# Kernel optimization log

Hardware: AMD Instinct MI355X
Metric: run time of the kernel (lower is better)

The kernel has to match this reference:

```python
import jax, jax.numpy as jnp
import numpy as np
jax.config.update("jax_enable_x64", True)

PAD_ID = -1
NUM_DISCRETE = 128  # args.n_discrete_size

def _lexsort3(v):
    # torch code: stable argsort by x, then y, then z -> final key order z (primary), y, x.
    # numpy/jax lexsort: last key is primary, and it is stable.
    idx = jnp.lexsort((v[:, 0], v[:, 1], v[:, 2]))
    return v[idx], idx

def setup_inputs() -> dict:
    key = jax.random.key(0)
    k1, k2 = jax.random.split(key)
    B, NV, NF = 32, 32768, 65536
    vertices = jax.random.normal(k1, (B, NV, 3), dtype=jnp.float32)
    faces = jax.random.randint(k2, (B, NF, 3), 0, NV, dtype=jnp.int64)
    n_pad = NF // 10
    faces = faces.at[:, NF - n_pad:, :].set(PAD_ID)
    return {"vertices": vertices, "faces": faces}

def reference(vertices, faces):
    B, NV, _ = vertices.shape
    # normalize_vertices reduces over dim 0 (which is the BATCH dim here) - faithful to source
    mn = vertices.min(axis=0)
    mx = vertices.max(axis=0)
    center = (mn + mx) * 0.5
    longest = (mx - mn).max()
    v = (vertices - center) / longest
    # batched lexicographic sort of vertices
    sorted_v, sort_idx = jax.vmap(_lexsort3)(v)
    # inverse permutation (inv[sort_idx] = arange  <=>  argsort of a permutation)
    inv = jnp.argsort(sort_idx, axis=1)  # (B, NV)
    # torch indexes inverse_mapping[faces] with pad -1 wrapping to NV-1
    wrapped = jnp.mod(faces, NV)
    reindexed = jax.vmap(lambda m, f: m[f])(inv, wrapped)  # (B, NF, 3)
    sorted_faces, _ = jax.vmap(_lexsort3)(reindexed)
    # face mask: all three vertex ids != pad
    face_mask = jnp.all(faces != PAD_ID, axis=-1)  # (B, NF)
    face_np = jnp.where(face_mask[..., None], faces, 0)
    # gather vertex coords per face: (B, NF, 3verts, 3coords). The torch code
    # materializes a (b,nf,nv,3) repeat then gathers; we gather directly.
    face_coords = jax.vmap(lambda vv, ff: vv[ff])(sorted_v, face_np)
    # discretize into [-1, 1] -> [0, 127]
    t = (face_coords + 1.0) * 0.5 * NUM_DISCRETE - 0.5
    dq = jnp.clip(jnp.round(t).astype(jnp.int64), 0, NUM_DISCRETE - 1)
    codes = jnp.where(face_mask[..., None, None], dq, PAD_ID)
    input_ids = codes.reshape(B, -1)
    attention_mask = (input_ids != PAD_ID).astype(jnp.float32)
    ph = jnp.full((B, 1), PAD_ID, dtype=input_ids.dtype)
    input_ids = jnp.concatenate([ph, input_ids, ph], axis=1)
    attention_mask = jnp.concatenate([ph.astype(jnp.float32), attention_mask, ph.astype(jnp.float32)], axis=1)
    return input_ids, attention_mask, codes, dq, sorted_faces
```

## Files before the change

kernel.cpp:

```cpp
#include <hip/hip_runtime.h>
#include <stdint.h>

#define BATCH 32
#define NV 32768
#define NF 65536
#define PCOUNT (NV*3)


__device__ __forceinline__ unsigned fenc(float f){
  unsigned u = __float_as_uint(f);
  return (u & 0x80000000u) ? ~u : (u | 0x80000000u);
}
__device__ __forceinline__ float fdec(unsigned e){
  unsigned u = (e & 0x80000000u) ? (e & 0x7FFFFFFFu) : ~e;
  return __uint_as_float(u);
}

__global__ void kminmax(const float* __restrict__ vert, float* __restrict__ center,
                        unsigned* __restrict__ longestBits){
  int p = blockIdx.x*256 + threadIdx.x;
  float mn = 3.4e38f, mx = -3.4e38f;
  #pragma unroll
  for (int b = 0; b < BATCH; ++b) {
    float v = vert[(size_t)b*PCOUNT + p];
    mn = fminf(mn, v); mx = fmaxf(mx, v);
  }
  center[p] = __fadd_rn(mn, mx) * 0.5f;
  float r = __fsub_rn(mx, mn);
  for (int off = 32; off > 0; off >>= 1) r = fmaxf(r, __shfl_down(r, off, 64));
  if ((threadIdx.x & 63) == 0) atomicMax(longestBits, __float_as_uint(r));
}

__device__ __forceinline__ bool less4(uint4 a, uint4 b){
  if (a.x != b.x) return a.x < b.x;
  if (a.y != b.y) return a.y < b.y;
  if (a.z != b.z) return a.z < b.z;
  return a.w < b.w;
}
__device__ __forceinline__ bool less2(uint2 a, uint2 b){
  if (a.y != b.y) return a.y < b.y;
  return a.x < b.x;
}

__device__ __forceinline__ int split64v(const uint4* __restrict__ A,
                                        const uint4* __restrict__ B,
                                        int k, int L){
  int lo = k - L; if (lo < 0) lo = 0;
  int hi = k < L ? k : L;
  int lane = threadIdx.x & 63;
  while (lo < hi){
    int n = hi - lo;
    int pos = lo + (int)(((long long)n * lane) >> 6);
    bool pred = less4(A[pos], B[k-1-pos]);
    unsigned long long m = __ballot(pred);
    int t = __popcll(m);
    if (t == 0){ hi = lo; break; }
    int pl = lo + (int)(((long long)n * (t-1)) >> 6);
    int nh = (t == 64) ? hi : (lo + (int)(((long long)n * t) >> 6));
    lo = pl + 1; hi = nh;
  }
  return lo;
}
__device__ __forceinline__ int split64f(const uint2* __restrict__ A,
                                        const uint2* __restrict__ B,
                                        int k, int L){
  int lo = k - L; if (lo < 0) lo = 0;
  int hi = k < L ? k : L;
  int lane = threadIdx.x & 63;
  while (lo < hi){
    int n = hi - lo;
    int pos = lo + (int)(((long long)n * lane) >> 6);
    bool pred = less2(A[pos], B[k-1-pos]);
    unsigned long long m = __ballot(pred);
    int t = __popcll(m);
    if (t == 0){ hi = lo; break; }
    int pl = lo + (int)(((long long)n * (t-1)) >> 6);
    int nh = (t == 64) ? hi : (lo + (int)(((long long)n * t) >> 6));
    lo = pl + 1; hi = nh;
  }
  return lo;
}

#define VT 4096
#define FT 8192
#define SWV(i) ((i) ^ (((i) >> 3) & 7))
#define SWF(i) ((i) ^ (((i) >> 4) & 15))

__global__ __launch_bounds__(1024) void klocalv(const float* __restrict__ vert,
                                                const float* __restrict__ center,
                                                const unsigned* __restrict__ longestBits,
                                                uint4* __restrict__ S){
  __shared__ uint4 sh[VT];
  int blockBase = blockIdx.x * VT;
  float L = __uint_as_float(*longestBits);
  float rl = __fdiv_rn(1.0f, L);
  for (int i = threadIdx.x; i < VT; i += 1024){
    int id = blockBase + i;
    int vi = id & (NV-1);
    size_t vb = (size_t)(id >> 15)*PCOUNT + (size_t)vi*3;
    float nx = __fsub_rn(vert[vb+0], center[vi*3+0]);
    float ny = __fsub_rn(vert[vb+1], center[vi*3+1]);
    float nz = __fsub_rn(vert[vb+2], center[vi*3+2]);
    float x = __fmul_rn(nx, rl);
    float y = __fmul_rn(ny, rl);
    float z = __fmul_rn(nz, rl);
    uint4 s; s.x = fenc(z); s.y = fenc(y); s.z = fenc(x); s.w = (unsigned)vi;
    sh[SWV(i)] = s;
  }
  __syncthreads();
  int t = threadIdx.x;
  int k0 = t * 4;
  uint4 v[4];
  #pragma unroll
  for (int e = 0; e < 4; ++e) v[e] = sh[SWV(k0 + e)];
  #pragma unroll
  for (int k = 2; k <= 4; k <<= 1){
    #pragma unroll
    for (int j = k >> 1; j > 0; j >>= 1){
      #pragma unroll
      for (int i = 0; i < 4; ++i){
        int l = i ^ j;
        if (l > i){
          bool up = ((i & k) == 0);
          bool sw = up ? less4(v[l], v[i]) : less4(v[i], v[l]);
          if (sw){ uint4 tmp = v[i]; v[i] = v[l]; v[l] = tmp; }
        }
      }
    }
  }
  #pragma unroll
  for (int e = 0; e < 4; ++e) sh[SWV(k0 + e)] = v[e];
  __syncthreads();
  for (int w = 4; w < VT; w <<= 1){
    int base = k0 & ~(2*w - 1);
    int ko = k0 - base;
    int lo = ko - w; if (lo < 0) lo = 0;
    int hi = ko < w ? ko : w;
    while (lo < hi){
      int mid = (lo + hi) >> 1;
      if (less4(sh[SWV(base + mid)], sh[SWV(base + w + ko-1-mid)])) lo = mid + 1; else hi = mid;
    }
    int i = lo, j = ko - lo;
    uint4 m[4];
    #pragma unroll
    for (int e = 0; e < 4; ++e){
      bool takeA = (j >= w) || (i < w && less4(sh[SWV(base + i)], sh[SWV(base + w + j)]));
      m[e] = takeA ? sh[SWV(base + i)] : sh[SWV(base + w + j)];
      if (takeA) ++i; else ++j;
    }
    __syncthreads();
    #pragma unroll
    for (int e = 0; e < 4; ++e) sh[SWV(k0 + e)] = m[e];
    __syncthreads();
  }
  uint4* basep = S + (size_t)blockBase;
  for (int i = threadIdx.x; i < VT; i += 1024) basep[i] = sh[SWV(i)];
}

__global__ __launch_bounds__(256) void kmergev(const uint4* __restrict__ src,
                                               uint4* __restrict__ dst, int L){
  __shared__ uint4 sh[1024];
  __shared__ int sAB[2];
  int gid = blockIdx.x;
  int b = gid >> 5, c = gid & 31;
  const uint4* base = src + ((size_t)b << 15);
  uint4* obase = dst + ((size_t)b << 15);
  int co = c * 1024;
  int pair = co / (2*L);
  int ko = co - pair*2*L;
  const uint4* A = base + (size_t)pair*2*L;
  const uint4* B = A + L;
  uint4* O = obase + (size_t)pair*2*L + ko;
  int wv = threadIdx.x >> 6;
  if (wv < 2){
    int s = split64v(A, B, ko + wv*1024, L);
    if ((threadIdx.x & 63) == 0) sAB[wv] = s;
  }
  __syncthreads();
  int aStart = sAB[0];
  int na = sAB[1] - aStart;
  int nb = 1024 - na;
  int bStart = ko - aStart;
  for (int i = threadIdx.x; i < 1024; i += 256)
    sh[i] = (i < na) ? A[aStart + i] : B[bStart + (i - na)];
  __syncthreads();
  int k0 = threadIdx.x * 4;
  int lo = k0 - nb; if (lo < 0) lo = 0;
  int hi = k0 < na ? k0 : na;
  while (lo < hi){
    int mid = (lo + hi) >> 1;
    if (less4(sh[mid], sh[na + k0-1-mid])) lo = mid + 1; else hi = mid;
  }
  int i = lo, j = k0 - lo;
  #pragma unroll
  for (int e = 0; e < 4; ++e){
    bool takeA = (j >= nb) || (i < na && less4(sh[i], sh[na + j]));
    uint4 v = takeA ? sh[i] : sh[na + j];
    if (takeA) ++i; else ++j;
    O[k0 + e] = v;
  }
}

__global__ __launch_bounds__(256) void kmergevQ(const uint4* __restrict__ src,
                                                int* __restrict__ inv,
                                                unsigned* __restrict__ Q){
  #pragma clang fp contract(off)
  __shared__ uint4 sh[1024];
  __shared__ int sAB[2];
  const int L = 16384;
  int gid = blockIdx.x;
  int b = gid >> 5, c = gid & 31;
  const uint4* A = src + ((size_t)b << 15);
  const uint4* B = A + L;
  int ko = c * 1024;
  int wv = threadIdx.x >> 6;
  if (wv < 2){
    int s = split64v(A, B, ko + wv*1024, L);
    if ((threadIdx.x & 63) == 0) sAB[wv] = s;
  }
  __syncthreads();
  int aStart = sAB[0];
  int na = sAB[1] - aStart;
  int nb = 1024 - na;
  int bStart = ko - aStart;
  for (int i = threadIdx.x; i < 1024; i += 256)
    sh[i] = (i < na) ? A[aStart + i] : B[bStart + (i - na)];
  __syncthreads();
  int k0 = threadIdx.x * 4;
  int lo = k0 - nb; if (lo < 0) lo = 0;
  int hi = k0 < na ? k0 : na;
  while (lo < hi){
    int mid = (lo + hi) >> 1;
    if (less4(sh[mid], sh[na + k0-1-mid])) lo = mid + 1; else hi = mid;
  }
  int i = lo, j = k0 - lo;
  #pragma unroll
  for (int e = 0; e < 4; ++e){
    bool takeA = (j >= nb) || (i < na && less4(sh[i], sh[na + j]));
    uint4 s = takeA ? sh[i] : sh[na + j];
    if (takeA) ++i; else ++j;
    int pos = ko + k0 + e;
    inv[(b<<15) + (int)s.w] = pos;
    float cco[3]; cco[0] = fdec(s.z); cco[1] = fdec(s.y); cco[2] = fdec(s.x);
    unsigned qw = 0;
    #pragma unroll
    for (int cc = 0; cc < 3; ++cc){
      float tt = ((cco[cc] + 1.0f) * 0.5f) * 128.0f - 0.5f;
      float rq = rintf(tt);
      int qi = (int)rq;
      qi = qi < 0 ? 0 : (qi > 127 ? 127 : qi);
      qw |= ((unsigned)qi) << (8*cc);
    }
    Q[(b<<15) + pos] = qw;
  }
}

__global__ __launch_bounds__(1024) void klocalfB(const int* __restrict__ faces,
                                                 const int* __restrict__ inv,
                                                 const unsigned* __restrict__ Qt,
                                                 uint2* __restrict__ F,
                                                 float* __restrict__ out){
  __shared__ __align__(16) uint2 sh[FT];
  float* shq = (float*)sh;
  float* shm = ((float*)sh) + 9216;
  int p = blockIdx.x;
  int l = ((p & 7) << 5) | (p >> 3);
  int blockBase = l * FT;
  int b = blockBase >> 16;
  const int* invb = inv + (b << 15);
  const unsigned* Qb = Qt + (b << 15);
  int t = threadIdx.x;
  uint2 v[8];
  #pragma unroll 8
  for (int c = 0; c < 8; ++c){
    int i = c*1024 + t;
    int id = blockBase + i;
    int f = id & (NF-1);
    size_t fb = (size_t)id*3;
    int f0 = faces[fb+0], f1 = faces[fb+1], f2 = faces[fb+2];
    bool mask = (f0 != -1) & (f1 != -1) & (f2 != -1);
    unsigned r0 = (unsigned)invb[f0 & (NV-1)];
    unsigned r1 = (unsigned)invb[f1 & (NV-1)];
    unsigned r2 = (unsigned)invb[f2 & (NV-1)];
    v[c].x = (r0 << 15) | (unsigned)f;
    v[c].y = (r2 << 15) | r1;
    unsigned qw0 = Qb[mask ? f0 : 0];
    unsigned qw1 = Qb[mask ? f1 : 0];
    unsigned qw2 = Qb[mask ? f2 : 0];
    shm[t] = mask ? 1.0f : 0.0f;
    shq[t*9+0] = (float)( qw0        & 255u);
    shq[t*9+1] = (float)((qw0 >> 8 ) & 255u);
    shq[t*9+2] = (float)((qw0 >> 16) & 255u);
    shq[t*9+3] = (float)( qw1        & 255u);
    shq[t*9+4] = (float)((qw1 >> 8 ) & 255u);
    shq[t*9+5] = (float)((qw1 >> 16) & 255u);
    shq[t*9+6] = (float)( qw2        & 255u);
    shq[t*9+7] = (float)((qw2 >> 8 ) & 255u);
    shq[t*9+8] = (float)((qw2 >> 16) & 255u);
    __syncthreads();
    float4* cp = (float4*)(out + 37748864 + ((size_t)blockBase + c*1024)*9);
    float4* dp = (float4*)(out + 56623232 + ((size_t)blockBase + c*1024)*9);
    for (int r = t; r < 2304; r += 1024){
      int e0 = r*4;
      float4 q = *(const float4*)&shq[e0];
      float m0 = shm[(unsigned)(e0  )/9u];
      float m1 = shm[(unsigned)(e0+1)/9u];
      float m2 = shm[(unsigned)(e0+2)/9u];
      float m3 = shm[(unsigned)(e0+3)/9u];
      float4 cv;
      cv.x = m0 != 0.0f ? q.x : -1.0f;
      cv.y = m1 != 0.0f ? q.y : -1.0f;
      cv.z = m2 != 0.0f ? q.z : -1.0f;
      cv.w = m3 != 0.0f ? q.w : -1.0f;
      cp[r] = cv;
      dp[r] = q;
    }
    size_t fi = (size_t)(blockBase & (NF-1)) + (size_t)c*1024;
    size_t idsBase  = (size_t)b*589826 + 1 + fi*9;
    size_t attnBase = 18874432 + idsBase;
    #pragma unroll
    for (int r = 0; r < 9; ++r){
      int idx = r*1024 + t;
      float q = shq[idx];
      float m = shm[(unsigned)idx/9u];
      out[idsBase + idx]  = m != 0.0f ? q : -1.0f;
      out[attnBase + idx] = m;
    }
    __syncthreads();
  }
  if ((blockBase & (NF-1)) == 0 && t == 0){
    out[(size_t)b*589826]                     = -1.0f;
    out[(size_t)b*589826 + 589825]            = -1.0f;
    out[18874432 + (size_t)b*589826]          = -1.0f;
    out[18874432 + (size_t)b*589826 + 589825] = -1.0f;
  }
  #pragma unroll
  for (int k = 2; k <= 8; k <<= 1){
    #pragma unroll
    for (int j = k >> 1; j > 0; j >>= 1){
      #pragma unroll
      for (int i = 0; i < 8; ++i){
        int l2 = i ^ j;
        if (l2 > i){
          bool up = ((i & k) == 0);
          bool sw = up ? less2(v[l2], v[i]) : less2(v[i], v[l2]);
          if (sw){ uint2 tmp = v[i]; v[i] = v[l2]; v[l2] = tmp; }
        }
      }
    }
  }
  int k0 = t * 8;
  #pragma unroll
  for (int e = 0; e < 8; ++e) sh[SWF(k0 + e)] = v[e];
  __syncthreads();
  for (int w = 8; w < FT; w <<= 1){
    int base = k0 & ~(2*w - 1);
    int ko = k0 - base;
    int lo = ko - w; if (lo < 0) lo = 0;
    int hi = ko < w ? ko : w;
    while (lo < hi){
      int mid = (lo + hi) >> 1;
      if (less2(sh[SWF(base + mid)], sh[SWF(base + w + ko-1-mid)])) lo = mid + 1; else hi = mid;
    }
    int i = lo, j = ko - lo;
    uint2 m[8];
    #pragma unroll
    for (int e = 0; e < 8; ++e){
      bool takeA = (j >= w) || (i < w && less2(sh[SWF(base + i)], sh[SWF(base + w + j)]));
      m[e] = takeA ? sh[SWF(base + i)] : sh[SWF(base + w + j)];
      if (takeA) ++i; else ++j;
    }
    __syncthreads();
    #pragma unroll
    for (int e = 0; e < 8; ++e) sh[SWF(k0 + e)] = m[e];
    __syncthreads();
  }
  uint2* basep = F + (size_t)blockBase;
  for (int i = threadIdx.x; i < FT; i += 1024) basep[i] = sh[SWF(i)];
}

__global__ __launch_bounds__(256) void kmergef(const uint2* __restrict__ src,
                                               uint2* __restrict__ dst, int L){
  __shared__ uint2 sh[1024];
  __shared__ int sAB[2];
  int gid = blockIdx.x;
  int b = gid >> 6, c = gid & 63;
  const uint2* base = src + ((size_t)b << 16);
  uint2* obase = dst + ((size_t)b << 16);
  int co = c * 1024;
  int pair = co / (2*L);
  int ko = co - pair*2*L;
  const uint2* A = base + (size_t)pair*2*L;
  const uint2* B = A + L;
  uint2* O = obase + (size_t)pair*2*L + ko;
  int wv = threadIdx.x >> 6;
  if (wv < 2){
    int s = split64f(A, B, ko + wv*1024, L);
    if ((threadIdx.x & 63) == 0) sAB[wv] = s;
  }
  __syncthreads();
  int aStart = sAB[0];
  int na = sAB[1] - aStart;
  int nb = 1024 - na;
  int bStart = ko - aStart;
  for (int i = threadIdx.x; i < 1024; i += 256)
    sh[i] = (i < na) ? A[aStart + i] : B[bStart + (i - na)];
  __syncthreads();
  int k0 = threadIdx.x * 4;
  int lo = k0 - nb; if (lo < 0) lo = 0;
  int hi = k0 < na ? k0 : na;
  while (lo < hi){
    int mid = (lo + hi) >> 1;
    if (less2(sh[mid], sh[na + k0-1-mid])) lo = mid + 1; else hi = mid;
  }
  int i = lo, j = k0 - lo;
  #pragma unroll
  for (int e = 0; e < 4; ++e){
    bool takeA = (j >= nb) || (i < na && less2(sh[i], sh[na + j]));
    uint2 v = takeA ? sh[i] : sh[na + j];
    if (takeA) ++i; else ++j;
    O[k0 + e] = v;
  }
}

__global__ __launch_bounds__(256) void kmergefOut(const uint2* __restrict__ src,
                                                  float* __restrict__ out){
  __shared__ __align__(16) float shf[3072];
  __shared__ int sAB[2];
  uint2* sh = (uint2*)shf;
  const int L = 32768;
  int gid = blockIdx.x;
  int b = gid >> 6, c = gid & 63;
  const uint2* A = src + ((size_t)b << 16);
  const uint2* B = A + L;
  int ko = c * 1024;
  int wv = threadIdx.x >> 6;
  if (wv < 2){
    int s = split64f(A, B, ko + wv*1024, L);
    if ((threadIdx.x & 63) == 0) sAB[wv] = s;
  }
  __syncthreads();
  int aStart = sAB[0];
  int na = sAB[1] - aStart;
  int nb = 1024 - na;
  int bStart = ko - aStart;
  for (int i = threadIdx.x; i < 1024; i += 256)
    sh[i] = (i < na) ? A[aStart + i] : B[bStart + (i - na)];
  __syncthreads();
  int k0 = threadIdx.x * 4;
  int lo = k0 - nb; if (lo < 0) lo = 0;
  int hi = k0 < na ? k0 : na;
  while (lo < hi){
    int mid = (lo + hi) >> 1;
    if (less2(sh[mid], sh[na + k0-1-mid])) lo = mid + 1; else hi = mid;
  }
  int i = lo, j = k0 - lo;
  uint2 v[4];
  #pragma unroll
  for (int e = 0; e < 4; ++e){
    bool takeA = (j >= nb) || (i < na && less2(sh[i], sh[na + j]));
    v[e] = takeA ? sh[i] : sh[na + j];
    if (takeA) ++i; else ++j;
  }
  __syncthreads();
  #pragma unroll
  for (int e = 0; e < 4; ++e){
    int o = (k0 + e) * 3;
    shf[o+0] = (float)(v[e].x >> 15);
    shf[o+1] = (float)(v[e].y & 0x7FFFu);
    shf[o+2] = (float)(v[e].y >> 15);
  }
  __syncthreads();
  size_t basef = 75497600 + ((size_t)b*65536 + (size_t)ko)*3;
  for (int q = threadIdx.x; q < 3072; q += 256) out[basef + q] = shf[q];
}

extern "C" void kernel_launch(void* const* d_in, const int* in_sizes, int n_in,
                              void* d_out, int out_size, void* d_ws, size_t ws_size,
                              hipStream_t stream){
  const float* vert  = (const float*)d_in[0];
  const int*   faces = (const int*)d_in[1];
  float* out = (float*)d_out;

  uint4*    S           = (uint4*)d_ws;
  uint4*    S2          = (uint4*)((char*)d_ws + 16777216);
  uint2*    FKa         = (uint2*)((char*)d_ws + 16777216);
  unsigned* Q           = (unsigned*)((char*)d_ws + 16777216);
  uint2*    FKb         = (uint2*)d_ws;
  int*      inv         = (int*)((char*)d_ws + 33554432);
  float*    center      = (float*)((char*)d_ws + 37748736);
  unsigned* longestBits = (unsigned*)((char*)d_ws + 38141952);

  hipMemsetAsync(longestBits, 0, 4, stream);
  kminmax<<<PCOUNT/256, 256, 0, stream>>>(vert, center, longestBits);

  klocalv<<<BATCH*(NV/VT), 1024, 0, stream>>>(vert, center, longestBits, S);
  kmergev<<<BATCH*32, 256, 0, stream>>>(S,  S2, 4096);
  kmergev<<<BATCH*32, 256, 0, stream>>>(S2, S,  8192);
  kmergevQ<<<BATCH*32, 256, 0, stream>>>(S, inv, Q);

  klocalfB<<<BATCH*(NF/FT), 1024, 0, stream>>>(faces, inv, Q, FKb, out);

  kmergef<<<BATCH*64, 256, 0, stream>>>(FKb, FKa, 8192);
  kmergef<<<BATCH*64, 256, 0, stream>>>(FKa, FKb, 16384);
  kmergefOut<<<BATCH*64, 256, 0, stream>>>(FKb, out);
}
```

Measured before the change: 595.1 us.

## Stage per-wave output chunks in LDS to drop block-wide barriers

Each wavefront now owns a private 640-float LDS slice and handles 64 contiguous faces per iteration, instead of the whole block sharing one staging buffer for 1024 faces. The two __syncthreads per chunk are replaced by an lgkmcnt wait and a scheduling barrier, because a wave only reads what it wrote itself. One barrier is added before the sort phase reuses the same LDS. This changes which faces each thread holds before the local sort and relies on wave-level ordering of LDS accesses, which is a correctness risk.

```diff
diff --git a/kernel.cpp b/kernel.cpp
--- a/kernel.cpp
+++ b/kernel.cpp
@@ -5,6 +5,8 @@
 #define NV 32768
 #define NF 65536
 #define PCOUNT (NV*3)
+
+typedef float f32x4 __attribute__((ext_vector_type(4)));
 
 
 __device__ __forceinline__ unsigned fenc(float f){
@@ -261,8 +263,6 @@
                                                  uint2* __restrict__ F,
                                                  float* __restrict__ out){
   __shared__ __align__(16) uint2 sh[FT];
-  float* shq = (float*)sh;
-  float* shm = ((float*)sh) + 9216;
   int p = blockIdx.x;
   int l = ((p & 7) << 5) | (p >> 3);
   int blockBase = l * FT;
@@ -270,10 +270,13 @@
   const int* invb = inv + (b << 15);
   const unsigned* Qb = Qt + (b << 15);
   int t = threadIdx.x;
+  int wv = t >> 6, ln = t & 63;
+  float* wq = ((float*)sh) + wv*640;
+  float* wm = wq + 576;
   uint2 v[8];
-  #pragma unroll 8
-  for (int c = 0; c < 8; ++c){
-    int i = c*1024 + t;
+  #pragma unroll
+  for (int e = 0; e < 8; ++e){
+    int i = wv*512 + e*64 + ln;
     int id = blockBase + i;
     int f = id & (NF-1);
     size_t fb = (size_t)id*3;
@@ -282,32 +285,34 @@
     unsigned r0 = (unsigned)invb[f0 & (NV-1)];
     unsigned r1 = (unsigned)invb[f1 & (NV-1)];
     unsigned r2 = (unsigned)invb[f2 & (NV-1)];
-    v[c].x = (r0 << 15) | (unsigned)f;
-    v[c].y = (r2 << 15) | r1;
+    v[e].x = (r0 << 15) | (unsigned)f;
+    v[e].y = (r2 << 15) | r1;
     unsigned qw0 = Qb[mask ? f0 : 0];
     unsigned qw1 = Qb[mask ? f1 : 0];
     unsigned qw2 = Qb[mask ? f2 : 0];
-    shm[t] = mask ? 1.0f : 0.0f;
-    shq[t*9+0] = (float)( qw0        & 255u);
-    shq[t*9+1] = (float)((qw0 >> 8 ) & 255u);
-    shq[t*9+2] = (float)((qw0 >> 16) & 255u);
-    shq[t*9+3] = (float)( qw1        & 255u);
-    shq[t*9+4] = (float)((qw1 >> 8 ) & 255u);
-    shq[t*9+5] = (float)((qw1 >> 16) & 255u);
-    shq[t*9+6] = (float)( qw2        & 255u);
-    shq[t*9+7] = (float)((qw2 >> 8 ) & 255u);
-    shq[t*9+8] = (float)((qw2 >> 16) & 255u);
-    __syncthreads();
-    float4* cp = (float4*)(out + 37748864 + ((size_t)blockBase + c*1024)*9);
-    float4* dp = (float4*)(out + 56623232 + ((size_t)blockBase + c*1024)*9);
-    for (int r = t; r < 2304; r += 1024){
+    wm[ln] = mask ? 1.0f : 0.0f;
+    wq[ln*9+0] = (float)( qw0        & 255u);
+    wq[ln*9+1] = (float)((qw0 >> 8 ) & 255u);
+    wq[ln*9+2] = (float)((qw0 >> 16) & 255u);
+    wq[ln*9+3] = (float)( qw1        & 255u);
+    wq[ln*9+4] = (float)((qw1 >> 8 ) & 255u);
+    wq[ln*9+5] = (float)((qw1 >> 16) & 255u);
+    wq[ln*9+6] = (float)( qw2        & 255u);
+    wq[ln*9+7] = (float)((qw2 >> 8 ) & 255u);
+    wq[ln*9+8] = (float)((qw2 >> 16) & 255u);
+    asm volatile("s_waitcnt lgkmcnt(0)" ::: "memory");
+    __builtin_amdgcn_sched_barrier(0);
+    size_t chunkF = (size_t)blockBase + (size_t)wv*512 + (size_t)e*64;
+    f32x4* cp = (f32x4*)(out + 37748864 + chunkF*9);
+    f32x4* dp = (f32x4*)(out + 56623232 + chunkF*9);
+    for (int r = ln; r < 144; r += 64){
       int e0 = r*4;
-      float4 q = *(const float4*)&shq[e0];
-      float m0 = shm[(unsigned)(e0  )/9u];
-      float m1 = shm[(unsigned)(e0+1)/9u];
-      float m2 = shm[(unsigned)(e0+2)/9u];
-      float m3 = shm[(unsigned)(e0+3)/9u];
-      float4 cv;
+      f32x4 q = *(const f32x4*)&wq[e0];
+      float m0 = wm[(unsigned)(e0  )/9u];
+      float m1 = wm[(unsigned)(e0+1)/9u];
+      float m2 = wm[(unsigned)(e0+2)/9u];
+      float m3 = wm[(unsigned)(e0+3)/9u];
+      f32x4 cv;
       cv.x = m0 != 0.0f ? q.x : -1.0f;
       cv.y = m1 != 0.0f ? q.y : -1.0f;
       cv.z = m2 != 0.0f ? q.z : -1.0f;
@@ -315,18 +320,17 @@
       cp[r] = cv;
       dp[r] = q;
     }
-    size_t fi = (size_t)(blockBase & (NF-1)) + (size_t)c*1024;
+    size_t fi = chunkF & (NF-1);
     size_t idsBase  = (size_t)b*589826 + 1 + fi*9;
     size_t attnBase = 18874432 + idsBase;
     #pragma unroll
     for (int r = 0; r < 9; ++r){
-      int idx = r*1024 + t;
-      float q = shq[idx];
-      float m = shm[(unsigned)idx/9u];
+      int idx = r*64 + ln;
+      float q = wq[idx];
+      float m = wm[(unsigned)idx/9u];
       out[idsBase + idx]  = m != 0.0f ? q : -1.0f;
       out[attnBase + idx] = m;
     }
-    __syncthreads();
   }
   if ((blockBase & (NF-1)) == 0 && t == 0){
     out[(size_t)b*589826]                     = -1.0f;
@@ -349,6 +353,7 @@
       }
     }
   }
+  __syncthreads();
   int k0 = t * 8;
   #pragma unroll
   for (int e = 0; e < 8; ++e) sh[SWF(k0 + e)] = v[e];
```

After: 629.6 us. 5.8% more time.
